# Performance work log

Hardware: AMD Instinct MI355X
Metric: run time of the kernel (lower is better)

The kernel has to match this reference:

```python
import math
import jax, jax.numpy as jnp
import numpy as np

B, LQ, LK, D, H = 4, 2048, 2048, 512, 8  # dim_Q=dim_K=dim_V=D, num_heads=H


def _layernorm(x, g, b, eps=1e-5):
    mu = jnp.mean(x, axis=-1, keepdims=True)
    var = jnp.var(x, axis=-1, keepdims=True)
    return (x - mu) * jax.lax.rsqrt(var + eps) * g + b


def setup_inputs() -> dict:
    key = jax.random.key(0)
    ks = jax.random.split(key, 16)
    s = 1.0 / math.sqrt(D)
    return {
        "Q": jax.random.normal(ks[0], (B, LQ, D), jnp.float32),
        "K": jax.random.normal(ks[1], (B, LK, D), jnp.float32),
        "pad_mask": jax.random.randint(ks[2], (B, LK), 0, 2, jnp.int32),
        "Wq": jax.random.normal(ks[3], (D, D), jnp.float32) * s,
        "bq": jnp.zeros((D,), jnp.float32),
        "Wk": jax.random.normal(ks[4], (D, D), jnp.float32) * s,
        "bk": jnp.zeros((D,), jnp.float32),
        "Wv": jax.random.normal(ks[5], (D, D), jnp.float32) * s,
        "bv": jnp.zeros((D,), jnp.float32),
        "Wo": jax.random.normal(ks[6], (D, D), jnp.float32) * s,
        "bo": jnp.zeros((D,), jnp.float32),
        "g0": jnp.ones((D,), jnp.float32),
        "b0": jnp.zeros((D,), jnp.float32),
        "g1": jnp.ones((D,), jnp.float32),
        "b1": jnp.zeros((D,), jnp.float32),
    }


def reference(Q, K, pad_mask, Wq, bq, Wk, bk, Wv, bv, Wo, bo, g0, b0, g1, b1):
    d = D // H  # head dim (torch: split(dim_split, 2) then cat along batch)
    Qh = (Q @ Wq + bq).reshape(B, LQ, H, d)
    Kh = (K @ Wk + bk).reshape(B, LK, H, d)
    Vh = (K @ Wv + bv).reshape(B, LK, H, d)
    # NOTE: original scales by sqrt(dim_V), not sqrt(head_dim)
    score = jnp.einsum('bqhd,bkhd->bhqk', Qh, Kh) / np.float32(math.sqrt(D))
    m = pad_mask[:, None, None, :].astype(score.dtype)  # (B,1,1,Lk)
    score = jnp.where(m == 0, jnp.float32(-1e12), score)
    A = jax.nn.softmax(score, axis=-1) * m  # post-softmax mask multiply (faithful)
    O = jnp.einsum('bhqk,bkhd->bqhd', A, Vh).reshape(B, LQ, D)
    O = Q + O
    O = _layernorm(O, g0, b0)
    O = O + jax.nn.relu(O @ Wo + bo)
    O = _layernorm(O, g1, b1)
    return O
```

## Files before the change

### kernel.cpp

```cpp
#include <hip/hip_runtime.h>
#include <math.h>

#define NB   4
#define SLQ  2048
#define SLK  2048
#define DIM  512
#define NH   8
#define HD   64
#define NROWS (NB * SLQ)
#define NT   (SLK / 64)

typedef __attribute__((ext_vector_type(8)))  __bf16 bf16x8;
typedef __attribute__((ext_vector_type(4)))  __bf16 bf16x4;
typedef __attribute__((ext_vector_type(2)))  __bf16 bf16x2;
typedef __attribute__((ext_vector_type(4)))  float  f32x4;
typedef __attribute__((ext_vector_type(16))) float  f32x16;
typedef __attribute__((ext_vector_type(4)))  unsigned int u32x4;

typedef const __attribute__((address_space(1))) void* as1_cptr;
typedef __attribute__((address_space(3))) void*       as3_ptr;
__device__ __forceinline__ void async_ld16(const void* g, void* s) {
    __builtin_amdgcn_global_load_lds((as1_cptr)g, (as3_ptr)s, 16, 0, 0);
}

__global__ __launch_bounds__(256)
void transpose_w_kernel(const float* __restrict__ Wq, const float* __restrict__ Wk,
                        const float* __restrict__ Wv, const float* __restrict__ Wo,
                        const int* __restrict__ maskp,
                        __bf16* __restrict__ Wt, float* __restrict__ msentg) {
    const int m = blockIdx.z;
    const int t = threadIdx.x;
    if (m == 4) {
        const int idx = (blockIdx.y * 16 + blockIdx.x) * 256 + t;
        if (idx < NB * SLK) msentg[idx] = maskp[idx] ? 0.f : -1e30f;
        return;
    }
    __shared__ float Ls[32][33];
    const float* W = (m == 0) ? Wq : (m == 1) ? Wk : (m == 2) ? Wv : Wo;
    const int k0 = blockIdx.y * 32, n0 = blockIdx.x * 32;
    const int r  = t >> 3, c = (t & 7) * 4;

    const float4 v = *reinterpret_cast<const float4*>(&W[(size_t)(k0 + r) * DIM + n0 + c]);
    Ls[r][c + 0] = v.x; Ls[r][c + 1] = v.y; Ls[r][c + 2] = v.z; Ls[r][c + 3] = v.w;
    __syncthreads();

    const int n = t >> 3, k = (t & 7) * 4;
    bf16x4 o;
    o[0] = (__bf16)Ls[k + 0][n];
    o[1] = (__bf16)Ls[k + 1][n];
    o[2] = (__bf16)Ls[k + 2][n];
    o[3] = (__bf16)Ls[k + 3][n];
    *reinterpret_cast<bf16x4*>(&Wt[(size_t)(512 * m + n0 + n) * DIM + k0 + k]) = o;
}

__global__ __launch_bounds__(256)
void proj_mfma_kernel(const float* __restrict__ Qp, const float* __restrict__ Kp,
                      const __bf16* __restrict__ Wt,
                      const float* __restrict__ bq, const float* __restrict__ bk,
                      const float* __restrict__ bv,
                      __bf16* __restrict__ Qh, __bf16* __restrict__ Kh,
                      __bf16* __restrict__ VhT) {
    __shared__ __bf16 As[2][128][64];
    __shared__ __bf16 Bs[2][128][64];

    const int pos  = blockIdx.x;
    const int orig = (pos & 7) * 96 + (pos >> 3);
    const int by   = orig / 12;
    const int bx   = orig % 12;
    const int mode = bx >> 2;
    const int cb   = bx & 3;
    const float*  Ag = (mode == 0) ? Qp : Kp;
    const __bf16* Bt = Wt + (size_t)(mode * 512) * DIM;
    const float*  biasp = ((mode == 0) ? bq : (mode == 1) ? bk : bv) + cb * 128;
    const int col0 = cb * 128;

    const int t  = threadIdx.x;
    const int w  = t >> 6, l = t & 63, lg = l >> 4, lc = l & 15;
    const int wr = w >> 1, wc = w & 1;
    const int row0 = by * 128;

    float biasr[4];
    #pragma unroll
    for (int nj = 0; nj < 4; ++nj) biasr[nj] = biasp[wc * 64 + nj * 16 + lc];
    asm volatile("s_waitcnt vmcnt(0)" ::: "memory");

    const int sr   = t >> 3;
    const int sc8  = t & 7;
    const int swA  = (sc8 ^ (sr & 7)) * 8;
    const int srow = l >> 3;
    const int schk = (l & 7) ^ srow;
    const int x7   = lc & 7;

    f32x4 acc[4][4];
    #pragma unroll
    for (int mi = 0; mi < 4; ++mi)
        #pragma unroll
        for (int nj = 0; nj < 4; ++nj) acc[mi][nj] = f32x4{0.f, 0.f, 0.f, 0.f};

    float4 areg[4][2];

#define PROJ_CF asm volatile("" ::: "memory")
#define PROJ_ISSUE_A(k0_) { _Pragma("unroll") for (int i = 0; i < 4; ++i) {    \
        const float* ap = Ag + (size_t)(row0 + i * 32 + sr) * DIM + (k0_) + sc8 * 8; \
        areg[i][0] = *reinterpret_cast<const float4*>(ap);                     \
        areg[i][1] = *reinterpret_cast<const float4*>(ap + 4); } PROJ_CF; }
#define PROJ_CVT(nb_) { _Pragma("unroll") for (int i = 0; i < 4; ++i) {        \
        bf16x8 hv;                                                             \
        hv[0] = (__bf16)areg[i][0].x; hv[1] = (__bf16)areg[i][0].y;            \
        hv[2] = (__bf16)areg[i][0].z; hv[3] = (__bf16)areg[i][0].w;            \
        hv[4] = (__bf16)areg[i][1].x; hv[5] = (__bf16)areg[i][1].y;            \
        hv[6] = (__bf16)areg[i][1].z; hv[7] = (__bf16)areg[i][1].w;            \
        *reinterpret_cast<bf16x8*>(&As[nb_][i * 32 + sr][swA]) = hv; } }
#define PROJ_STAGE_B(nb_, k0_) { _Pragma("unroll") for (int i = 0; i < 4; ++i) { \
        const int rb = w * 32 + i * 8;                                         \
        async_ld16(Bt + (size_t)(col0 + rb + srow) * DIM + (k0_) + schk * 8,   \
                   &Bs[nb_][rb][0]); } PROJ_CF; }

    PROJ_ISSUE_A(0);
    asm volatile("s_waitcnt vmcnt(0)" ::: "memory");
    PROJ_CVT(0);
    PROJ_STAGE_B(0, 0);
    PROJ_ISSUE_A(64);
    asm volatile("s_waitcnt vmcnt(8)" ::: "memory");
    asm volatile("s_waitcnt lgkmcnt(0)" ::: "memory");
    __builtin_amdgcn_s_barrier();

    for (int kt = 0; kt < 8; ++kt) {
        const int cur = kt & 1;
        if (kt + 1 < 8) PROJ_STAGE_B((kt + 1) & 1, (kt + 1) * 64);

        #pragma unroll
        for (int ks = 0; ks < 2; ++ks) {
            bf16x8 af[4], bfv[4];
            #pragma unroll
            for (int mi = 0; mi < 4; ++mi)
                af[mi] = *reinterpret_cast<const bf16x8*>(
                    &As[cur][wr * 64 + mi * 16 + lc][((ks * 4 + lg) ^ x7) << 3]);
            #pragma unroll
            for (int nj = 0; nj < 4; ++nj)
                bfv[nj] = *reinterpret_cast<const bf16x8*>(
                    &Bs[cur][wc * 64 + nj * 16 + lc][((ks * 4 + lg) ^ x7) << 3]);
            #pragma unroll
            for (int mi = 0; mi < 4; ++mi)
                #pragma unroll
                for (int nj = 0; nj < 4; ++nj)
                    acc[mi][nj] = __builtin_amdgcn_mfma_f32_16x16x32_bf16(
                        af[mi], bfv[nj], acc[mi][nj], 0, 0, 0);
        }

        if (kt + 1 < 8) {
            asm volatile("s_waitcnt vmcnt(4)" ::: "memory");
            PROJ_CVT((kt + 1) & 1);
            if (kt + 2 < 8) {
                PROJ_ISSUE_A((kt + 2) * 64);
                asm volatile("s_waitcnt vmcnt(8)" ::: "memory");
            } else {
                asm volatile("s_waitcnt vmcnt(0)" ::: "memory");
            }
            asm volatile("s_waitcnt lgkmcnt(0)" ::: "memory");
            __builtin_amdgcn_s_barrier();
        }
    }

    #pragma unroll
    for (int mi = 0; mi < 4; ++mi) {
        #pragma unroll
        for (int nj = 0; nj < 4; ++nj) {
            const int cl  = wc * 64 + nj * 16 + lc;
            const float bb = biasr[nj];
            if (mode == 2) {
                const int dcol = col0 + cl;
                const int hh = dcol >> 6, dd = dcol & 63;
                const int row = row0 + wr * 64 + mi * 16 + lg * 4;
                const int bi  = row >> 11, key = row & 2047;
                bf16x4 pk;
                #pragma unroll
                for (int r = 0; r < 4; ++r) pk[r] = (__bf16)(acc[mi][nj][r] + bb);
                *reinterpret_cast<bf16x4*>(
                    &VhT[((size_t)(bi * NH + hh) * HD + dd) * SLK + key]) = pk;
            } else {
                __bf16* out = (mode == 0) ? Qh : Kh;
                #pragma unroll
                for (int r = 0; r < 4; ++r) {
                    const int row = row0 + wr * 64 + mi * 16 + lg * 4 + r;
                    out[(size_t)row * DIM + col0 + cl] = (__bf16)(acc[mi][nj][r] + bb);
                }
            }
        }
    }
}

__global__ __launch_bounds__(256)
void ffn_mfma_kernel(const __bf16* __restrict__ A, const __bf16* __restrict__ Bt,
                     const float* __restrict__ bias, __bf16* __restrict__ outv) {
    __shared__ __bf16 As[128][72];
    __shared__ __bf16 Bs[64][72];

    const int pos  = blockIdx.x;
    const int orig = (pos & 7) * 64 + (pos >> 3);
    const int by   = orig >> 3;
    const int bxc  = orig & 7;

    const int t  = threadIdx.x;
    const int w  = t >> 6, l = t & 63, lg = l >> 4, lc = l & 15;
    const int wr = w >> 1, wc = w & 1;
    const int row0 = by * 128, col0 = bxc * 64;

    f32x4 acc[4][2];
    #pragma unroll
    for (int mi = 0; mi < 4; ++mi)
        #pragma unroll
        for (int nj = 0; nj < 2; ++nj) acc[mi][nj] = f32x4{0.f, 0.f, 0.f, 0.f};

    const int sr = t >> 3, sc = (t & 7) * 8;

    for (int k0 = 0; k0 < DIM; k0 += 64) {
        __syncthreads();
        #pragma unroll
        for (int i = 0; i < 4; ++i) {
            const int r = i * 32 + sr;
            *reinterpret_cast<bf16x8*>(&As[r][sc]) =
                *reinterpret_cast<const bf16x8*>(&A[(size_t)(row0 + r) * DIM + k0 + sc]);
        }
        #pragma unroll
        for (int i = 0; i < 2; ++i) {
            const int n = i * 32 + sr;
            *reinterpret_cast<bf16x8*>(&Bs[n][sc]) =
                *reinterpret_cast<const bf16x8*>(&Bt[(size_t)(col0 + n) * DIM + k0 + sc]);
        }
        __syncthreads();

        #pragma unroll
        for (int ks = 0; ks < 2; ++ks) {
            bf16x8 af[4], bfv[2];
            #pragma unroll
            for (int mi = 0; mi < 4; ++mi)
                af[mi] = *reinterpret_cast<const bf16x8*>(
                    &As[wr * 64 + mi * 16 + lc][ks * 32 + lg * 8]);
            #pragma unroll
            for (int nj = 0; nj < 2; ++nj)
                bfv[nj] = *reinterpret_cast<const bf16x8*>(
                    &Bs[wc * 32 + nj * 16 + lc][ks * 32 + lg * 8]);
            #pragma unroll
            for (int mi = 0; mi < 4; ++mi)
                #pragma unroll
                for (int nj = 0; nj < 2; ++nj)
                    acc[mi][nj] = __builtin_amdgcn_mfma_f32_16x16x32_bf16(
                        af[mi], bfv[nj], acc[mi][nj], 0, 0, 0);
        }
    }

    #pragma unroll
    for (int mi = 0; mi < 4; ++mi) {
        #pragma unroll
        for (int nj = 0; nj < 2; ++nj) {
            const int cl  = wc * 32 + nj * 16 + lc;
            const int col = col0 + cl;
            #pragma unroll
            for (int r = 0; r < 4; ++r) {
                const int row = row0 + wr * 64 + mi * 16 + lg * 4 + r;
                const float vv = acc[mi][nj][r] + bias[col];
                outv[(size_t)row * DIM + col] =
                    (__bf16)((float)A[(size_t)row * DIM + col] + fmaxf(vv, 0.f));
            }
        }
    }
}

__global__ __launch_bounds__(256)
void attn_mfma_kernel(const __bf16* __restrict__ Qh, const __bf16* __restrict__ Kh,
                      const __bf16* __restrict__ VhT, const float* __restrict__ msentg,
                      __bf16* __restrict__ Oa) {
    const int pos  = blockIdx.x;
    const int orig = (pos & 7) * 64 + (pos >> 3);
    const int qb = orig & 15;
    const int h  = (orig >> 4) & 7;
    const int b  = orig >> 7;

    const int tid = threadIdx.x;
    const int w   = tid >> 6;
    const int l   = tid & 63;
    const int ql  = l & 31;
    const int hi  = l >> 5;
    const int x7  = ql & 7;

    __shared__ __bf16 Ks[3][64][64];
    __shared__ __bf16 Vt[3][64][64];
    __shared__ float  msent[SLK];
    __shared__ float  linv[4][32];

    {
        const float* mb = msentg + b * SLK;
        #pragma unroll
        for (int i = 0; i < 2; ++i) {
            const int idx = (i * 256 + tid) * 4;
            *reinterpret_cast<f32x4*>(&msent[idx]) =
                *reinterpret_cast<const f32x4*>(&mb[idx]);
        }
    }

    const int q0 = qb * 128 + w * 32;
    bf16x8 qf[4];
    {
        const __bf16* qrow = Qh + (size_t)(b * SLQ + q0 + ql) * DIM + h * HD + hi * 8;
        #pragma unroll
        for (int c = 0; c < 4; ++c)
            qf[c] = *reinterpret_cast<const bf16x8*>(qrow + c * 16);
    }

    const __bf16* kbase = Kh  + (size_t)b * SLK * DIM + h * HD;
    const __bf16* vbase = VhT + (size_t)(b * NH + h) * HD * SLK;

    const int srow = l >> 3;
    const int schk = (l & 7) ^ srow;

    auto STAGE = [&](int nb_, int k0_) {
        #pragma unroll
        for (int i = 0; i < 2; ++i) {
            const int rb = w * 16 + i * 8;
            async_ld16(kbase + (size_t)(k0_ + rb + srow) * DIM + schk * 8,
                       &Ks[nb_][rb][0]);
            async_ld16(vbase + (size_t)(rb + srow) * SLK + k0_ + schk * 8,
                       &Vt[nb_][rb][0]);
        }
    };

    f32x16 oacc[2];
    #pragma unroll
    for (int i = 0; i < 16; ++i) { oacc[0][i] = 0.f; oacc[1][i] = 0.f; }
    float l_part = 0.f;
    const float scale2 = 0.06377551f;

    STAGE(0, 0);
    STAGE(1, 64);
    asm volatile("s_waitcnt lgkmcnt(0)" ::: "memory");

    int rd = 0;
    for (int t = 0; t < NT; ++t) {
        if (t == NT - 1) asm volatile("s_waitcnt vmcnt(0)" ::: "memory");
        else             asm volatile("s_waitcnt vmcnt(4)" ::: "memory");
        __builtin_amdgcn_s_barrier();

        if (t + 2 < NT) {
            const int st = (rd + 2 >= 3) ? rd - 1 : rd + 2;
            STAGE(st, (t + 2) * 64);
        }

        const int k0 = t * 64;
        const __bf16* KsC = &Ks[rd][0][0];
        const __bf16* VtC = &Vt[rd][0][0];

        f32x16 sacc[2];
        #pragma unroll
        for (int i = 0; i < 16; ++i) { sacc[0][i] = 0.f; sacc[1][i] = 0.f; }
        __builtin_amdgcn_s_setprio(1);
        #pragma unroll
        for (int kb = 0; kb < 2; ++kb) {
            #pragma unroll
            for (int c = 0; c < 4; ++c) {
                const bf16x8 kf = *reinterpret_cast<const bf16x8*>(
                    &KsC[(kb * 32 + ql) * 64 + (((2 * c + hi) ^ x7) << 3)]);
                sacc[kb] = __builtin_amdgcn_mfma_f32_32x32x16_bf16(
                    kf, qf[c], sacc[kb], 0, 0, 0);
            }
        }
        __builtin_amdgcn_s_setprio(0);

        unsigned int P2[2][8];
        #pragma unroll
        for (int kb = 0; kb < 2; ++kb) {
            #pragma unroll
            for (int m = 0; m < 4; ++m) {
                const f32x4 tm = *reinterpret_cast<const f32x4*>(
                    &msent[k0 + kb * 32 + 8 * m + 4 * hi]);
                float p[4];
                #pragma unroll
                for (int j = 0; j < 4; ++j) {
                    p[j] = __builtin_amdgcn_exp2f(
                        fmaf(sacc[kb][4 * m + j], scale2, tm[j]));
                    l_part += p[j];
                }
                bf16x2 w0, w1;
                w0[0] = (__bf16)p[0]; w0[1] = (__bf16)p[1];
                w1[0] = (__bf16)p[2]; w1[1] = (__bf16)p[3];
                P2[kb][2 * m]     = __builtin_bit_cast(unsigned int, w0);
                P2[kb][2 * m + 1] = __builtin_bit_cast(unsigned int, w1);
            }
        }

        #pragma unroll
        for (int kb = 0; kb < 2; ++kb) {
            #pragma unroll
            for (int cc = 0; cc < 2; ++cc) {
                asm volatile("v_permlane32_swap_b32 %0, %1"
                             : "+v"(P2[kb][4 * cc + 0]), "+v"(P2[kb][4 * cc + 2]));
                asm volatile("v_permlane32_swap_b32 %0, %1"
                             : "+v"(P2[kb][4 * cc + 1]), "+v"(P2[kb][4 * cc + 3]));
            }
        }
        bf16x8 pfrag[4];
        #pragma unroll
        for (int c = 0; c < 4; ++c) {
            const int kb = c >> 1, cc = c & 1;
            u32x4 fw;
            fw.x = P2[kb][4 * cc + 0]; fw.y = P2[kb][4 * cc + 1];
            fw.z = P2[kb][4 * cc + 2]; fw.w = P2[kb][4 * cc + 3];
            pfrag[c] = __builtin_bit_cast(bf16x8, fw);
        }

        __builtin_amdgcn_s_setprio(1);
        #pragma unroll
        for (int db = 0; db < 2; ++db) {
            #pragma unroll
            for (int c = 0; c < 4; ++c) {
                const bf16x8 vf = *reinterpret_cast<const bf16x8*>(
                    &VtC[(db * 32 + ql) * 64 + (((2 * c + hi) ^ x7) << 3)]);
                oacc[db] = __builtin_amdgcn_mfma_f32_32x32x16_bf16(
                    pfrag[c], vf, oacc[db], 0, 0, 0);
            }
        }
        __builtin_amdgcn_s_setprio(0);

        rd = (rd == 2) ? 0 : rd + 1;
    }

    const float lsum = l_part + __shfl_xor(l_part, 32, 64);
    if (hi == 0) linv[w][ql] = (lsum > 0.f) ? 1.f / lsum : 0.f;
    #pragma unroll
    for (int db = 0; db < 2; ++db) {
        #pragma unroll
        for (int m = 0; m < 4; ++m) {
            const f32x4 iv = *reinterpret_cast<const f32x4*>(&linv[w][8 * m + 4 * hi]);
            #pragma unroll
            for (int j = 0; j < 4; ++j) {
                const int qr = 8 * m + 4 * hi + j;
                Oa[(size_t)(b * SLQ + q0 + qr) * DIM + h * HD + db * 32 + ql] =
                    (__bf16)(oacc[db][4 * m + j] * iv[j]);
            }
        }
    }
}

__device__ __forceinline__ float wave_sum(float v) {
    #pragma unroll
    for (int off = 32; off > 0; off >>= 1) v += __shfl_xor(v, off, 64);
    return v;
}

__global__ __launch_bounds__(256)
void ln1_kernel(const __bf16* X, const float* Y,
                const float* g, const float* bta, __bf16* out) {
    const int w    = threadIdx.x >> 6;
    const int lane = threadIdx.x & 63;
    const int row  = blockIdx.x * 4 + w;
    const size_t base = (size_t)row * DIM + lane * 8;

    const bf16x8 xv = *reinterpret_cast<const bf16x8*>(&X[base]);
    const float4 y0 = *reinterpret_cast<const float4*>(&Y[base]);
    const float4 y1 = *reinterpret_cast<const float4*>(&Y[base + 4]);
    float v[8];
    v[0] = (float)xv[0] + y0.x; v[1] = (float)xv[1] + y0.y;
    v[2] = (float)xv[2] + y0.z; v[3] = (float)xv[3] + y0.w;
    v[4] = (float)xv[4] + y1.x; v[5] = (float)xv[5] + y1.y;
    v[6] = (float)xv[6] + y1.z; v[7] = (float)xv[7] + y1.w;

    float s = 0.f, ss = 0.f;
    #pragma unroll
    for (int i = 0; i < 8; ++i) { s += v[i]; ss += v[i] * v[i]; }
    s  = wave_sum(s);
    ss = wave_sum(ss);
    const float mean = s * (1.f / DIM);
    const float var  = ss * (1.f / DIM) - mean * mean;
    const float rstd = rsqrtf(var + 1e-5f);

    const float4 g0 = *reinterpret_cast<const float4*>(&g[lane * 8]);
    const float4 g1 = *reinterpret_cast<const float4*>(&g[lane * 8 + 4]);
    const float4 b0 = *reinterpret_cast<const float4*>(&bta[lane * 8]);
    const float4 b1 = *reinterpret_cast<const float4*>(&bta[lane * 8 + 4]);
    float gg[8] = {g0.x, g0.y, g0.z, g0.w, g1.x, g1.y, g1.z, g1.w};
    float bb[8] = {b0.x, b0.y, b0.z, b0.w, b1.x, b1.y, b1.z, b1.w};

    bf16x8 o;
    #pragma unroll
    for (int i = 0; i < 8; ++i)
        o[i] = (__bf16)((v[i] - mean) * rstd * gg[i] + bb[i]);
    *reinterpret_cast<bf16x8*>(&out[base]) = o;
}

__global__ __launch_bounds__(256)
void ln2_kernel(const __bf16* X, const float* g, const float* bta, float* out) {
    const int w    = threadIdx.x >> 6;
    const int lane = threadIdx.x & 63;
    const int row  = blockIdx.x * 4 + w;
    const size_t base = (size_t)row * DIM + lane * 8;

    const bf16x8 xv = *reinterpret_cast<const bf16x8*>(&X[base]);
    float v[8];
    #pragma unroll
    for (int i = 0; i < 8; ++i) v[i] = (float)xv[i];

    float s = 0.f, ss = 0.f;
    #pragma unroll
    for (int i = 0; i < 8; ++i) { s += v[i]; ss += v[i] * v[i]; }
    s  = wave_sum(s);
    ss = wave_sum(ss);
    const float mean = s * (1.f / DIM);
    const float var  = ss * (1.f / DIM) - mean * mean;
    const float rstd = rsqrtf(var + 1e-5f);

    const float4 g0 = *reinterpret_cast<const float4*>(&g[lane * 8]);
    const float4 g1 = *reinterpret_cast<const float4*>(&g[lane * 8 + 4]);
    const float4 b0 = *reinterpret_cast<const float4*>(&bta[lane * 8]);
    const float4 b1 = *reinterpret_cast<const float4*>(&bta[lane * 8 + 4]);
    float gg[8] = {g0.x, g0.y, g0.z, g0.w, g1.x, g1.y, g1.z, g1.w};
    float bb[8] = {b0.x, b0.y, b0.z, b0.w, b1.x, b1.y, b1.z, b1.w};

    float4 o0, o1;
    o0.x = (v[0] - mean) * rstd * gg[0] + bb[0];
    o0.y = (v[1] - mean) * rstd * gg[1] + bb[1];
    o0.z = (v[2] - mean) * rstd * gg[2] + bb[2];
    o0.w = (v[3] - mean) * rstd * gg[3] + bb[3];
    o1.x = (v[4] - mean) * rstd * gg[4] + bb[4];
    o1.y = (v[5] - mean) * rstd * gg[5] + bb[5];
    o1.z = (v[6] - mean) * rstd * gg[6] + bb[6];
    o1.w = (v[7] - mean) * rstd * gg[7] + bb[7];
    *reinterpret_cast<float4*>(&out[base])     = o0;
    *reinterpret_cast<float4*>(&out[base + 4]) = o1;
}

extern "C" void kernel_launch(void* const* d_in, const int* in_sizes, int n_in,
                              void* d_out, int out_size, void* d_ws, size_t ws_size,
                              hipStream_t stream) {
    const float* Q     = (const float*)d_in[0];
    const float* K     = (const float*)d_in[1];
    const int*   maskp = (const int*)  d_in[2];
    const float* Wq    = (const float*)d_in[3];
    const float* bq    = (const float*)d_in[4];
    const float* Wk    = (const float*)d_in[5];
    const float* bk    = (const float*)d_in[6];
    const float* Wv    = (const float*)d_in[7];
    const float* bv    = (const float*)d_in[8];
    const float* Wo    = (const float*)d_in[9];
    const float* bo    = (const float*)d_in[10];
    const float* g0    = (const float*)d_in[11];
    const float* b0    = (const float*)d_in[12];
    const float* g1    = (const float*)d_in[13];
    const float* b1    = (const float*)d_in[14];

    float* out = (float*)d_out;
    char*  ws  = (char*)d_ws;
    __bf16* Qh     = (__bf16*)ws;
    __bf16* Kh     = (__bf16*)(ws + (8u  << 20));
    __bf16* VhT    = (__bf16*)(ws + (16u << 20));
    __bf16* Wt     = (__bf16*)(ws + (24u << 20));
    __bf16* Oa     = (__bf16*)(ws + (26u << 20));
    __bf16* H1     = (__bf16*)(ws + (34u << 20));
    float*  msentg = (float*)(ws + (42u << 20));
    __bf16* R2     = (__bf16*)ws;

    transpose_w_kernel<<<dim3(16, 16, 5), 256, 0, stream>>>(
        Wq, Wk, Wv, Wo, maskp, Wt, msentg);

    proj_mfma_kernel<<<dim3(768), 256, 0, stream>>>(
        Q, K, Wt, bq, bk, bv, Qh, Kh, VhT);

    attn_mfma_kernel<<<dim3(512), 256, 0, stream>>>(Qh, Kh, VhT, msentg, Oa);

    ln1_kernel<<<NROWS / 4, 256, 0, stream>>>(Oa, Q, g0, b0, H1);

    ffn_mfma_kernel<<<dim3(512), 256, 0, stream>>>(
        H1, Wt + (size_t)1536 * DIM, bo, R2);

    ln2_kernel<<<NROWS / 4, 256, 0, stream>>>(R2, g1, b1, out);
}
```

Baseline: 122.9 us.

## Halve attention block size, double-buffer K/V, bf16 mask, fuse residual into attention

The attention kernel now uses 128 threads (2 waves) covering 64 query rows per block, and launches 1024 blocks instead of 512. K/V staging drops from a triple buffer to a double buffer with a full vmcnt(0) wait each iteration, and the mask sentinel array is stored in bf16 to cut LDS use. The Q residual add moves from ln1 into the attention epilogue, so ln1 no longer reads Q. The aim is more blocks and higher occupancy and less ln1 traffic. The cost is less prefetch depth and more redundant K/V loads per query row.

```diff
diff --git a/kernel.cpp b/kernel.cpp
--- a/kernel.cpp
+++ b/kernel.cpp
@@ -27,12 +27,13 @@
 void transpose_w_kernel(const float* __restrict__ Wq, const float* __restrict__ Wk,
                         const float* __restrict__ Wv, const float* __restrict__ Wo,
                         const int* __restrict__ maskp,
-                        __bf16* __restrict__ Wt, float* __restrict__ msentg) {
+                        __bf16* __restrict__ Wt, __bf16* __restrict__ msentg) {
     const int m = blockIdx.z;
     const int t = threadIdx.x;
     if (m == 4) {
         const int idx = (blockIdx.y * 16 + blockIdx.x) * 256 + t;
-        if (idx < NB * SLK) msentg[idx] = maskp[idx] ? 0.f : -1e30f;
+        if (idx < NB * SLK)
+            msentg[idx] = maskp[idx] ? (__bf16)0.f : (__bf16)(-1e30f);
         return;
     }
     __shared__ float Ls[32][33];
@@ -267,15 +268,15 @@
     }
 }
 
-__global__ __launch_bounds__(256)
+__global__ __launch_bounds__(128)
 void attn_mfma_kernel(const __bf16* __restrict__ Qh, const __bf16* __restrict__ Kh,
-                      const __bf16* __restrict__ VhT, const float* __restrict__ msentg,
-                      __bf16* __restrict__ Oa) {
+                      const __bf16* __restrict__ VhT, const __bf16* __restrict__ msentg,
+                      const float* __restrict__ Qres, __bf16* __restrict__ Oa) {
     const int pos  = blockIdx.x;
-    const int orig = (pos & 7) * 64 + (pos >> 3);
-    const int qb = orig & 15;
-    const int h  = (orig >> 4) & 7;
-    const int b  = orig >> 7;
+    const int orig = (pos & 7) * 128 + (pos >> 3);
+    const int qb = orig & 31;
+    const int h  = (orig >> 5) & 7;
+    const int b  = orig >> 8;
 
     const int tid = threadIdx.x;
     const int w   = tid >> 6;
@@ -284,22 +285,20 @@
     const int hi  = l >> 5;
     const int x7  = ql & 7;
 
-    __shared__ __bf16 Ks[3][64][64];
-    __shared__ __bf16 Vt[3][64][64];
-    __shared__ float  msent[SLK];
-    __shared__ float  linv[4][32];
+    __shared__ __bf16 Ks[2][64][64];
+    __shared__ __bf16 Vt[2][64][64];
+    __shared__ __bf16 msent[SLK];
+    __shared__ float  linv[2][32];
 
     {
-        const float* mb = msentg + b * SLK;
-        #pragma unroll
-        for (int i = 0; i < 2; ++i) {
-            const int idx = (i * 256 + tid) * 4;
-            *reinterpret_cast<f32x4*>(&msent[idx]) =
-                *reinterpret_cast<const f32x4*>(&mb[idx]);
-        }
-    }
-
-    const int q0 = qb * 128 + w * 32;
+        const __bf16* mb = msentg + b * SLK;
+        *reinterpret_cast<bf16x8*>(&msent[tid * 16]) =
+            *reinterpret_cast<const bf16x8*>(&mb[tid * 16]);
+        *reinterpret_cast<bf16x8*>(&msent[tid * 16 + 8]) =
+            *reinterpret_cast<const bf16x8*>(&mb[tid * 16 + 8]);
+    }
+
+    const int q0 = qb * 64 + w * 32;
     bf16x8 qf[4];
     {
         const __bf16* qrow = Qh + (size_t)(b * SLQ + q0 + ql) * DIM + h * HD + hi * 8;
@@ -316,8 +315,8 @@
 
     auto STAGE = [&](int nb_, int k0_) {
         #pragma unroll
-        for (int i = 0; i < 2; ++i) {
-            const int rb = w * 16 + i * 8;
+        for (int i = 0; i < 4; ++i) {
+            const int rb = w * 32 + i * 8;
             async_ld16(kbase + (size_t)(k0_ + rb + srow) * DIM + schk * 8,
                        &Ks[nb_][rb][0]);
             async_ld16(vbase + (size_t)(rb + srow) * SLK + k0_ + schk * 8,
@@ -332,23 +331,16 @@
     const float scale2 = 0.06377551f;
 
     STAGE(0, 0);
-    STAGE(1, 64);
     asm volatile("s_waitcnt lgkmcnt(0)" ::: "memory");
 
-    int rd = 0;
     for (int t = 0; t < NT; ++t) {
-        if (t == NT - 1) asm volatile("s_waitcnt vmcnt(0)" ::: "memory");
-        else             asm volatile("s_waitcnt vmcnt(4)" ::: "memory");
+        asm volatile("s_waitcnt vmcnt(0)" ::: "memory");
         __builtin_amdgcn_s_barrier();
-
-        if (t + 2 < NT) {
-            const int st = (rd + 2 >= 3) ? rd - 1 : rd + 2;
-            STAGE(st, (t + 2) * 64);
-        }
+        if (t + 1 < NT) STAGE((t + 1) & 1, (t + 1) * 64);
 
         const int k0 = t * 64;
-        const __bf16* KsC = &Ks[rd][0][0];
-        const __bf16* VtC = &Vt[rd][0][0];
+        const __bf16* KsC = &Ks[t & 1][0][0];
+        const __bf16* VtC = &Vt[t & 1][0][0];
 
         f32x16 sacc[2];
         #pragma unroll
@@ -371,13 +363,13 @@
         for (int kb = 0; kb < 2; ++kb) {
             #pragma unroll
             for (int m = 0; m < 4; ++m) {
-                const f32x4 tm = *reinterpret_cast<const f32x4*>(
+                const bf16x4 tmb = *reinterpret_cast<const bf16x4*>(
                     &msent[k0 + kb * 32 + 8 * m + 4 * hi]);
                 float p[4];
                 #pragma unroll
                 for (int j = 0; j < 4; ++j) {
                     p[j] = __builtin_amdgcn_exp2f(
-                        fmaf(sacc[kb][4 * m + j], scale2, tm[j]));
+                        fmaf(sacc[kb][4 * m + j], scale2, (float)tmb[j]));
                     l_part += p[j];
                 }
                 bf16x2 w0, w1;
@@ -420,8 +412,6 @@
             }
         }
         __builtin_amdgcn_s_setprio(0);
-
-        rd = (rd == 2) ? 0 : rd + 1;
     }
 
     const float lsum = l_part + __shfl_xor(l_part, 32, 64);
@@ -434,8 +424,8 @@
             #pragma unroll
             for (int j = 0; j < 4; ++j) {
                 const int qr = 8 * m + 4 * hi + j;
-                Oa[(size_t)(b * SLQ + q0 + qr) * DIM + h * HD + db * 32 + ql] =
-                    (__bf16)(oacc[db][4 * m + j] * iv[j]);
+                const size_t idx = (size_t)(b * SLQ + q0 + qr) * DIM + h * HD + db * 32 + ql;
+                Oa[idx] = (__bf16)(oacc[db][4 * m + j] * iv[j] + Qres[idx]);
             }
         }
     }
@@ -448,21 +438,16 @@
 }
 
 __global__ __launch_bounds__(256)
-void ln1_kernel(const __bf16* X, const float* Y,
-                const float* g, const float* bta, __bf16* out) {
+void ln1_kernel(const __bf16* X, const float* g, const float* bta, __bf16* out) {
     const int w    = threadIdx.x >> 6;
     const int lane = threadIdx.x & 63;
     const int row  = blockIdx.x * 4 + w;
     const size_t base = (size_t)row * DIM + lane * 8;
 
     const bf16x8 xv = *reinterpret_cast<const bf16x8*>(&X[base]);
-    const float4 y0 = *reinterpret_cast<const float4*>(&Y[base]);
-    const float4 y1 = *reinterpret_cast<const float4*>(&Y[base + 4]);
     float v[8];
-    v[0] = (float)xv[0] + y0.x; v[1] = (float)xv[1] + y0.y;
-    v[2] = (float)xv[2] + y0.z; v[3] = (float)xv[3] + y0.w;
-    v[4] = (float)xv[4] + y1.x; v[5] = (float)xv[5] + y1.y;
-    v[6] = (float)xv[6] + y1.z; v[7] = (float)xv[7] + y1.w;
+    #pragma unroll
+    for (int i = 0; i < 8; ++i) v[i] = (float)xv[i];
 
     float s = 0.f, ss = 0.f;
     #pragma unroll
@@ -555,7 +540,7 @@
     __bf16* Wt     = (__bf16*)(ws + (24u << 20));
     __bf16* Oa     = (__bf16*)(ws + (26u << 20));
     __bf16* H1     = (__bf16*)(ws + (34u << 20));
-    float*  msentg = (float*)(ws + (42u << 20));
+    __bf16* msentg = (__bf16*)(ws + (42u << 20));
     __bf16* R2     = (__bf16*)ws;
 
     transpose_w_kernel<<<dim3(16, 16, 5), 256, 0, stream>>>(
@@ -564,9 +549,10 @@
     proj_mfma_kernel<<<dim3(768), 256, 0, stream>>>(
         Q, K, Wt, bq, bk, bv, Qh, Kh, VhT);
 
-    attn_mfma_kernel<<<dim3(512), 256, 0, stream>>>(Qh, Kh, VhT, msentg, Oa);
-
-    ln1_kernel<<<NROWS / 4, 256, 0, stream>>>(Oa, Q, g0, b0, H1);
+    attn_mfma_kernel<<<dim3(1024), 128, 0, stream>>>(
+        Qh, Kh, VhT, msentg, Q, Oa);
+
+    ln1_kernel<<<NROWS / 4, 256, 0, stream>>>(Oa, g0, b0, H1);
 
     ffn_mfma_kernel<<<dim3(512), 256, 0, stream>>>(
         H1, Wt + (size_t)1536 * DIM, bo, R2);
```

Result: slower. 129.1 us (+5.1%).
